# Kernel optimization log

Measured on AMD Instinct MI355X. Metric: run time of the kernel, lower is better.

## Reference

```python
import jax, jax.numpy as jnp
import numpy as np

TAU = 2.0          # LIF membrane time constant
V_THRESHOLD = 1.0  # spikingjelly LIFNode default
V_RESET = 0.0      # hard reset target (spikingjelly default)
ATAN_ALPHA = 2.0   # surrogate.ATan default alpha

T, B, L, D_IN, D_OUT = 16, 32, 128, 512, 512


@jax.custom_vjp
def atan_spike(x):
    # Heaviside forward; ATan surrogate gradient in backward.
    return (x >= 0.0).astype(x.dtype)

def _atan_spike_fwd(x):
    return atan_spike(x), x

def _atan_spike_bwd(x, g):
    # d/dx [ (1/pi) * atan(pi/2 * alpha * x) + 1/2 ]
    grad = (ATAN_ALPHA / 2.0) / (1.0 + (jnp.pi / 2.0 * ATAN_ALPHA * x) ** 2)
    return (g * grad,)

atan_spike.defvjp(_atan_spike_fwd, _atan_spike_bwd)


def lif_multistep(h):
    """Multi-step LIF over leading time axis. h: [T, B, L, H] -> spikes [T, B, L, H].
    spikingjelly LIFNode (decay_input=True, hard reset, detach_reset=True):
      v = v + (x - (v - v_reset)) / tau
      s = heaviside(v - v_threshold)   (ATan surrogate grad)
      v = v_reset * s_detached + v * (1 - s_detached)
    """
    def step(v, x_t):
        v = v + (x_t - (v - V_RESET)) / TAU
        s = atan_spike(v - V_THRESHOLD)
        s_d = jax.lax.stop_gradient(s)  # detach_reset=True
        v = V_RESET * s_d + v * (1.0 - s_d)
        return v, s

    v0 = jnp.zeros_like(h[0])
    _, spikes = jax.lax.scan(step, v0, h)
    return spikes


def setup_inputs() -> dict:
    key = jax.random.key(0)
    kx, kw, kb = jax.random.split(key, 3)
    x = jax.random.normal(kx, (T, B, L, D_IN), dtype=jnp.float32)
    # nn.Linear init: U(-1/sqrt(fan_in), 1/sqrt(fan_in))
    bound = 1.0 / np.sqrt(D_IN)
    W = jax.random.uniform(kw, (D_OUT, D_IN), minval=-bound, maxval=bound, dtype=jnp.float32)
    b = jax.random.uniform(kb, (D_OUT,), minval=-bound, maxval=bound, dtype=jnp.float32)
    return {"x": x, "W": W, "b": b}


def reference(x, W, b):
    # Linear over flattened (T*B) dims == per-element projection, then LIF.
    h = jnp.einsum("tbld,hd->tblh", x, W) + b  # [T, B, L, D_OUT]
    return lif_multistep(h)
```

## Files before the change

kernel.cpp:

```cpp
#include <hip/hip_runtime.h>

using f32x4 = __attribute__((ext_vector_type(4))) float;
using s16x8 = __attribute__((ext_vector_type(8))) short;

constexpr int T_STEPS = 16;
constexpr int BLTOT   = 4096;
constexpr int KDIM    = 512;
constexpr int NDIM    = 512;

constexpr size_t B_BYTES = 32ull * 16 * 3 * 1024;
constexpr size_t A_BYTES = 512ull * 8 * 16 * 3 * 1024;
constexpr size_t ABASE   = B_BYTES;
constexpr size_t WS_NEED = A_BYTES + B_BYTES;


__device__ __forceinline__ void split8(const float* e, uint4& hp, uint4& mp, uint4& lp) {
  unsigned h[8], m[8], l[8];
#pragma unroll
  for (int j = 0; j < 8; ++j) {
    const float f = e[j];
    const unsigned u = __float_as_uint(f);
    h[j] = u >> 16;
    const float r1 = f - __uint_as_float(u & 0xFFFF0000u);
    const unsigned u1 = __float_as_uint(r1);
    m[j] = u1 >> 16;
    const float r2 = r1 - __uint_as_float(u1 & 0xFFFF0000u);
    l[j] = __float_as_uint(r2) >> 16;
  }
  hp = make_uint4(h[0] | (h[1] << 16), h[2] | (h[3] << 16),
                  h[4] | (h[5] << 16), h[6] | (h[7] << 16));
  mp = make_uint4(m[0] | (m[1] << 16), m[2] | (m[3] << 16),
                  m[4] | (m[5] << 16), m[6] | (m[7] << 16));
  lp = make_uint4(l[0] | (l[1] << 16), l[2] | (l[3] << 16),
                  l[4] | (l[5] << 16), l[6] | (l[7] << 16));
}

__global__ void split_w(const float* __restrict__ W, char* __restrict__ ws) {
  const int tid = threadIdx.x;
  const int wid = blockIdx.x * 4 + (tid >> 6);
  const int lane = tid & 63;
  const int nt = wid >> 4, ks = wid & 15;
  const int q = lane & 15, g = lane >> 4;
  const float* src = W + (size_t)(nt * 16 + q) * KDIM + ks * 32 + g * 8;
  float e[8];
  *(float4*)&e[0] = *(const float4*)src;
  *(float4*)&e[4] = *(const float4*)(src + 4);
  uint4 hp, mp, lp;
  split8(e, hp, mp, lp);
  char* dst = ws + (size_t)wid * 3072 + lane * 16;
  *(uint4*)(dst)        = hp;
  *(uint4*)(dst + 1024) = mp;
  *(uint4*)(dst + 2048) = lp;
}

__global__ void split_x(const float* __restrict__ x, char* __restrict__ ws) {
  const int tid = threadIdx.x;
  const int wid = blockIdx.x * 4 + (tid >> 6);
  const int lane = tid & 63;
  const int ks = wid & 15, mtile = wid >> 4;
  const int mt = mtile & 7, mb = mtile >> 3;
  const int q = lane & 15, g = lane >> 4;
  const int t  = (mt & 3) * 4 + (q & 3);
  const int bl = mb * 8 + (mt >> 2) * 4 + (q >> 2);
  const float* src = x + (size_t)(t * BLTOT + bl) * KDIM + ks * 32 + g * 8;
  float e[8];
  *(float4*)&e[0] = *(const float4*)src;
  *(float4*)&e[4] = *(const float4*)(src + 4);
  uint4 hp, mp, lp;
  split8(e, hp, mp, lp);
  char* dst = ws + ABASE + (size_t)wid * 3072 + lane * 16;
  *(uint4*)(dst)        = hp;
  *(uint4*)(dst + 1024) = mp;
  *(uint4*)(dst + 2048) = lp;
}

__global__ __launch_bounds__(256, 2)
void gemm_lif_frag(const char* __restrict__ wsB, const char* __restrict__ wsA,
                   const float* __restrict__ bias, float* __restrict__ out) {
  __shared__ __align__(16) char lds[48 * 1024];

  const int tid  = threadIdx.x;
  const int lane = tid & 63;
  const int wv   = tid >> 6;
  const int wm   = wv >> 1, wn = wv & 1;

  const int w    = blockIdx.x;
  const int orig = (w & 7) * 256 + (w >> 3);
  const int nb   = orig & 3;
  const int mb   = orig >> 2;

  const bool isA = (wv < 2);
  const int blk0 = isA ? (mb * 8 + wv * 4) : (nb * 8 + (wv - 2) * 4);
  const char* gbase = (isA ? wsA : wsB) + (size_t)blk0 * 49152 + lane * 16;
  char* ldsdst = lds + wv * 12288;

  f32x4 acc[4][4];
#pragma unroll
  for (int a = 0; a < 4; ++a)
#pragma unroll
    for (int b = 0; b < 4; ++b) acc[a][b] = (f32x4)(0.0f);

  int koff = 0;
  for (int ksl = 0; ksl < 16; ++ksl) {
#pragma unroll
    for (int i = 0; i < 12; ++i) {
      const int co = ((i / 3) * 48 + (i % 3)) * 1024;
      __builtin_amdgcn_global_load_lds(
          (const __attribute__((address_space(1))) void*)(gbase + koff + co),
          (__attribute__((address_space(3))) void*)(ldsdst + i * 1024), 16, 0, 0);
    }
    koff += 3072;
    __syncthreads();

    s16x8 bf[4][3];
#pragma unroll
    for (int nf = 0; nf < 4; ++nf)
#pragma unroll
      for (int c = 0; c < 3; ++c)
        bf[nf][c] = *(const s16x8*)(lds + 24576 + ((wn * 4 + nf) * 3 + c) * 1024 + lane * 16);

#pragma unroll
    for (int mf = 0; mf < 4; ++mf) {
      s16x8 af[3];
#pragma unroll
      for (int c = 0; c < 3; ++c)
        af[c] = *(const s16x8*)(lds + ((wm * 4 + mf) * 3 + c) * 1024 + lane * 16);
#pragma unroll
      for (int nf = 0; nf < 4; ++nf) {
        f32x4 c0 = acc[mf][nf];
        c0 = __builtin_amdgcn_mfma_f32_16x16x32_bf16(af[2], bf[nf][0], c0, 0, 0, 0);
        c0 = __builtin_amdgcn_mfma_f32_16x16x32_bf16(af[0], bf[nf][2], c0, 0, 0, 0);
        c0 = __builtin_amdgcn_mfma_f32_16x16x32_bf16(af[1], bf[nf][1], c0, 0, 0, 0);
        c0 = __builtin_amdgcn_mfma_f32_16x16x32_bf16(af[1], bf[nf][0], c0, 0, 0, 0);
        c0 = __builtin_amdgcn_mfma_f32_16x16x32_bf16(af[0], bf[nf][1], c0, 0, 0, 0);
        c0 = __builtin_amdgcn_mfma_f32_16x16x32_bf16(af[0], bf[nf][0], c0, 0, 0, 0);
        acc[mf][nf] = c0;
      }
    }
    __syncthreads();
  }

  const int G   = lane >> 4;
  const int bl  = mb * 8 + wm * 4 + G;
  const int col = lane & 15;
  const int n0  = nb * 128;
#pragma unroll
  for (int nf = 0; nf < 4; ++nf) {
    const int n = n0 + wn * 64 + nf * 16 + col;
    const float bb = bias[n];
    float v = 0.0f;
#pragma unroll
    for (int t = 0; t < T_STEPS; ++t) {
      const float h = ((const float*)&acc[t >> 2][nf])[t & 3] + bb;
      const float vn = v + (h - v) * 0.5f;
      const bool s = (vn >= 1.0f);
      out[(size_t)(t * BLTOT + bl) * NDIM + n] = s ? 1.0f : 0.0f;
      v = s ? 0.0f : vn;
    }
  }
}

constexpr int FB_ROWB  = 80;
constexpr int FB_COMP  = 128 * FB_ROWB;
constexpr int FB_BBASE = 3 * FB_COMP;

__device__ __forceinline__ void split3_write(char* lds, float4 v, int off) {
  unsigned u[4], u1[4], u2[4];
#pragma unroll
  for (int e = 0; e < 4; ++e) {
    float ve = ((const float*)&v)[e];
    u[e]  = __float_as_uint(ve);
    float r1 = ve - __uint_as_float(u[e] & 0xFFFF0000u);
    u1[e] = __float_as_uint(r1);
    float r2 = r1 - __uint_as_float(u1[e] & 0xFFFF0000u);
    u2[e] = __float_as_uint(r2);
  }
  uint2 hp, mp, lp;
  hp.x = (u[0]  >> 16) | (u[1]  & 0xFFFF0000u);
  hp.y = (u[2]  >> 16) | (u[3]  & 0xFFFF0000u);
  mp.x = (u1[0] >> 16) | (u1[1] & 0xFFFF0000u);
  mp.y = (u1[2] >> 16) | (u1[3] & 0xFFFF0000u);
  lp.x = (u2[0] >> 16) | (u2[1] & 0xFFFF0000u);
  lp.y = (u2[2] >> 16) | (u2[3] & 0xFFFF0000u);
  *(uint2*)(lds + off)               = hp;
  *(uint2*)(lds + off + FB_COMP)     = mp;
  *(uint2*)(lds + off + 2 * FB_COMP) = lp;
}

__global__ __launch_bounds__(256, 2)
void fused_mfma_lif_fb(const float* __restrict__ x, const float* __restrict__ W,
                       const float* __restrict__ bias, float* __restrict__ out) {
  __shared__ __align__(16) char lds[6 * FB_COMP];
  const int tid = threadIdx.x;
  const int lane = tid & 63;
  const int wv = tid >> 6, wm = wv >> 1, wn = wv & 1;
  const int bl0 = blockIdx.x * 8, n0 = blockIdx.y * 128;

  const float* aptr[4]; const float* bptr[4];
  int aw[4], bw[4];
#pragma unroll
  for (int i = 0; i < 4; ++i) {
    int f = i * 256 + tid, r = f >> 3, kq = (f & 7) * 4;
    int t = ((r >> 4) & 3) * 4 + (r & 3);
    int bl = (r >> 6) * 4 + ((r >> 2) & 3);
    aptr[i] = x + (size_t)(t * BLTOT + bl0 + bl) * KDIM + kq;
    bptr[i] = W + (size_t)(n0 + r) * KDIM + kq;
    aw[i] = r * FB_ROWB + kq * 2;
    bw[i] = FB_BBASE + r * FB_ROWB + kq * 2;
  }
  f32x4 acc[4][4];
#pragma unroll
  for (int a = 0; a < 4; ++a)
#pragma unroll
    for (int b = 0; b < 4; ++b) acc[a][b] = (f32x4)(0.0f);

  const int arow = (wm * 64 + (lane & 15)) * FB_ROWB + (lane >> 4) * 16;
  const int brow = FB_BBASE + (wn * 64 + (lane & 15)) * FB_ROWB + (lane >> 4) * 16;

  float4 ar[4], br[4];
#pragma unroll
  for (int i = 0; i < 4; ++i) { ar[i] = *(const float4*)(aptr[i]); br[i] = *(const float4*)(bptr[i]); }

  for (int it = 0; it < 16; ++it) {
    __syncthreads();
#pragma unroll
    for (int i = 0; i < 4; ++i) { split3_write(lds, ar[i], aw[i]); split3_write(lds, br[i], bw[i]); }
    __syncthreads();
    if (it < 15) {
      const int ko = (it + 1) * 32;
#pragma unroll
      for (int i = 0; i < 4; ++i) { ar[i] = *(const float4*)(aptr[i] + ko); br[i] = *(const float4*)(bptr[i] + ko); }
    }
    s16x8 bf[4][3];
#pragma unroll
    for (int nf = 0; nf < 4; ++nf)
#pragma unroll
      for (int c = 0; c < 3; ++c)
        bf[nf][c] = *(const s16x8*)(lds + brow + nf * 16 * FB_ROWB + c * FB_COMP);
#pragma unroll
    for (int mf = 0; mf < 4; ++mf) {
      s16x8 af[3];
#pragma unroll
      for (int c = 0; c < 3; ++c)
        af[c] = *(const s16x8*)(lds + arow + mf * 16 * FB_ROWB + c * FB_COMP);
#pragma unroll
      for (int nf = 0; nf < 4; ++nf) {
        f32x4 c0 = acc[mf][nf];
        c0 = __builtin_amdgcn_mfma_f32_16x16x32_bf16(af[2], bf[nf][0], c0, 0, 0, 0);
        c0 = __builtin_amdgcn_mfma_f32_16x16x32_bf16(af[0], bf[nf][2], c0, 0, 0, 0);
        c0 = __builtin_amdgcn_mfma_f32_16x16x32_bf16(af[1], bf[nf][1], c0, 0, 0, 0);
        c0 = __builtin_amdgcn_mfma_f32_16x16x32_bf16(af[1], bf[nf][0], c0, 0, 0, 0);
        c0 = __builtin_amdgcn_mfma_f32_16x16x32_bf16(af[0], bf[nf][1], c0, 0, 0, 0);
        c0 = __builtin_amdgcn_mfma_f32_16x16x32_bf16(af[0], bf[nf][0], c0, 0, 0, 0);
        acc[mf][nf] = c0;
      }
    }
  }
  const int G = lane >> 4, col = lane & 15;
  const int bl = bl0 + wm * 4 + G;
#pragma unroll
  for (int nf = 0; nf < 4; ++nf) {
    const int n = n0 + wn * 64 + nf * 16 + col;
    const float bb = bias[n];
    float v = 0.0f;
#pragma unroll
    for (int t = 0; t < T_STEPS; ++t) {
      const float h = ((const float*)&acc[t >> 2][nf])[t & 3] + bb;
      const float vn = v + (h - v) * 0.5f;
      const bool s = (vn >= 1.0f);
      out[(size_t)(t * BLTOT + bl) * NDIM + n] = s ? 1.0f : 0.0f;
      v = s ? 0.0f : vn;
    }
  }
}

extern "C" void kernel_launch(void* const* d_in, const int* in_sizes, int n_in,
                              void* d_out, int out_size, void* d_ws, size_t ws_size,
                              hipStream_t stream) {
  const float* x = (const float*)d_in[0];
  const float* W = (const float*)d_in[1];
  const float* b = (const float*)d_in[2];
  float* out = (float*)d_out;

  if (ws_size >= WS_NEED) {
    char* ws = (char*)d_ws;
    split_w<<<128, 256, 0, stream>>>(W, ws);
    split_x<<<16384, 256, 0, stream>>>(x, ws);
    gemm_lif_frag<<<2048, 256, 0, stream>>>(ws, ws + ABASE, b, out);
  } else {
    dim3 grid(BLTOT / 8, NDIM / 128);
    fused_mfma_lif_fb<<<grid, 256, 0, stream>>>(x, W, b, out);
  }
}
```

Before: 415.1 us.

## Stage x split through LDS for coalesced loads and raise GEMM occupancy

Replaces the per-wave split_x kernel with split_x2. Each block reads a full 16-row m-tile of x with contiguous float4 loads, splits it into three bf16 planes in padded shared memory, and writes the fragment-ordered layout out as contiguous 16-byte stores. This targets the strided, poorly coalesced global reads of the old split kernel. It also raises the GEMM kernel's launch-bounds occupancy hint from 2 to 3, which may force register spills.

```diff
diff --git a/kernel.cpp b/kernel.cpp
--- a/kernel.cpp
+++ b/kernel.cpp
@@ -33,6 +33,24 @@
                   m[4] | (m[5] << 16), m[6] | (m[7] << 16));
   lp = make_uint4(l[0] | (l[1] << 16), l[2] | (l[3] << 16),
                   l[4] | (l[5] << 16), l[6] | (l[7] << 16));
+}
+
+__device__ __forceinline__ void split4(const float4 v, uint2& hp, uint2& mp, uint2& lp) {
+  unsigned h[4], m[4], l[4];
+#pragma unroll
+  for (int j = 0; j < 4; ++j) {
+    const float f = ((const float*)&v)[j];
+    const unsigned u = __float_as_uint(f);
+    h[j] = u >> 16;
+    const float r1 = f - __uint_as_float(u & 0xFFFF0000u);
+    const unsigned u1 = __float_as_uint(r1);
+    m[j] = u1 >> 16;
+    const float r2 = r1 - __uint_as_float(u1 & 0xFFFF0000u);
+    l[j] = __float_as_uint(r2) >> 16;
+  }
+  hp = make_uint2(h[0] | (h[1] << 16), h[2] | (h[3] << 16));
+  mp = make_uint2(m[0] | (m[1] << 16), m[2] | (m[3] << 16));
+  lp = make_uint2(l[0] | (l[1] << 16), l[2] | (l[3] << 16));
 }
 
 __global__ void split_w(const float* __restrict__ W, char* __restrict__ ws) {
@@ -53,28 +71,48 @@
   *(uint4*)(dst + 2048) = lp;
 }
 
-__global__ void split_x(const float* __restrict__ x, char* __restrict__ ws) {
-  const int tid = threadIdx.x;
-  const int wid = blockIdx.x * 4 + (tid >> 6);
-  const int lane = tid & 63;
-  const int ks = wid & 15, mtile = wid >> 4;
+constexpr int XSTR   = 1040;
+constexpr int XPLANE = 16 * XSTR;
+
+__global__ __launch_bounds__(256)
+void split_x2(const float* __restrict__ x, char* __restrict__ ws) {
+  __shared__ __align__(16) char lds[3 * XPLANE];
+  const int tid   = threadIdx.x;
+  const int mtile = blockIdx.x;
   const int mt = mtile & 7, mb = mtile >> 3;
-  const int q = lane & 15, g = lane >> 4;
-  const int t  = (mt & 3) * 4 + (q & 3);
-  const int bl = mb * 8 + (mt >> 2) * 4 + (q >> 2);
-  const float* src = x + (size_t)(t * BLTOT + bl) * KDIM + ks * 32 + g * 8;
-  float e[8];
-  *(float4*)&e[0] = *(const float4*)src;
-  *(float4*)&e[4] = *(const float4*)(src + 4);
-  uint4 hp, mp, lp;
-  split8(e, hp, mp, lp);
-  char* dst = ws + ABASE + (size_t)wid * 3072 + lane * 16;
-  *(uint4*)(dst)        = hp;
-  *(uint4*)(dst + 1024) = mp;
-  *(uint4*)(dst + 2048) = lp;
-}
-
-__global__ __launch_bounds__(256, 2)
+
+#pragma unroll
+  for (int it = 0; it < 8; ++it) {
+    const int f   = it * 256 + tid;
+    const int q   = f >> 7;
+    const int col = f & 127;
+    const int t   = (mt & 3) * 4 + (q & 3);
+    const int bl  = mb * 8 + (mt >> 2) * 4 + (q >> 2);
+    const float4 v = *(const float4*)(x + (size_t)(t * BLTOT + bl) * KDIM + col * 4);
+    uint2 hp, mp, lp;
+    split4(v, hp, mp, lp);
+    char* base = lds + q * XSTR + col * 8;
+    *(uint2*)(base)              = hp;
+    *(uint2*)(base + XPLANE)     = mp;
+    *(uint2*)(base + 2 * XPLANE) = lp;
+  }
+  __syncthreads();
+
+  char* dstbase = ws + ABASE + (size_t)mtile * 49152;
+#pragma unroll
+  for (int it = 0; it < 12; ++it) {
+    const int d    = it * 256 + tid;
+    const int ks   = d / 192;
+    const int rem  = d - ks * 192;
+    const int cp   = rem >> 6;
+    const int lane = rem & 63;
+    const int q = lane & 15, g = lane >> 4;
+    const uint4 v = *(const uint4*)(lds + cp * XPLANE + q * XSTR + ks * 64 + g * 16);
+    *(uint4*)(dstbase + (size_t)d * 16) = v;
+  }
+}
+
+__global__ __launch_bounds__(256, 3)
 void gemm_lif_frag(const char* __restrict__ wsB, const char* __restrict__ wsA,
                    const float* __restrict__ bias, float* __restrict__ out) {
   __shared__ __align__(16) char lds[48 * 1024];
@@ -285,7 +323,7 @@
   if (ws_size >= WS_NEED) {
     char* ws = (char*)d_ws;
     split_w<<<128, 256, 0, stream>>>(W, ws);
-    split_x<<<16384, 256, 0, stream>>>(x, ws);
+    split_x2<<<4096, 256, 0, stream>>>(x, ws);
     gemm_lif_frag<<<2048, 256, 0, stream>>>(ws, ws + ABASE, b, out);
   } else {
     dim3 grid(BLTOT / 8, NDIM / 128);
```

After: 423.2 us. Within noise of the previous version (+1.9%).
